# Kernel optimization log

Hardware: AMD Instinct MI355X
Metric: run time of the kernel (lower is better)

## Reference

```python
import jax, jax.numpy as jnp
import numpy as np

N_NODES = 10000
N_EDGES = 160000
D_IN = 50
ALPHA = 0.2  # LeakyReLU negative slope


def _xavier(key, shape):
    fan_in, fan_out = shape[0], int(np.prod(shape[1:]))
    limit = float(np.sqrt(6.0 / (fan_in + fan_out)))
    return jax.random.uniform(key, shape, jnp.float32, -limit, limit)


def setup_inputs() -> dict:
    key = jax.random.key(0)
    ks = jax.random.split(key, 8)
    x = jax.random.normal(ks[0], (N_NODES, D_IN), jnp.float32)
    edge_idx = jax.random.randint(ks[1], (2, N_EDGES), 0, N_NODES, jnp.int64)
    # layer 1: 50 -> 4 heads x 256, concat
    W1 = _xavier(ks[2], (D_IN, 4, 256))
    a1 = _xavier(ks[3], (4, 512))  # [H, 2F]: split into a_src, a_dst
    # layer 2: 1024 -> 4 heads x 256, concat
    W2 = _xavier(ks[4], (1024, 4, 256))
    a2 = _xavier(ks[5], (4, 512))
    # layer 3: 1024 -> 6 heads x 121, mean
    W3 = _xavier(ks[6], (1024, 6, 121))
    a3 = _xavier(ks[7], (6, 242))
    return {"x": x, "edge_idx": edge_idx, "W1": W1, "a1": a1,
            "W2": W2, "a2": a2, "W3": W3, "a3": a3}


def gat_layer(h, W, a, src, dst, aggregate):
    """Multi-head GAT layer over an edge list. h:[N,Din], W:[Din,H,F], a:[H,2F]."""
    N = h.shape[0]
    Wh = jnp.einsum('nd,dhf->nhf', h, W)                    # [N, H, F]
    F = Wh.shape[-1]
    att_src = jnp.einsum('nhf,hf->nh', Wh, a[:, :F])         # a^T [Wh_i || .]
    att_dst = jnp.einsum('nhf,hf->nh', Wh, a[:, F:])         # a^T [. || Wh_j]
    logits = jax.nn.leaky_relu(att_src[src] + att_dst[dst], ALPHA)  # [E, H]
    # numerically stable softmax over incoming edges of each destination node
    m = jax.ops.segment_max(logits, dst, num_segments=N)
    e = jnp.exp(logits - m[dst])
    denom = jax.ops.segment_sum(e, dst, num_segments=N)
    coef = e / (denom[dst] + 1e-16)                           # [E, H]
    out = jax.ops.segment_sum(coef[:, :, None] * Wh[src], dst, num_segments=N)
    if aggregate == 'concat':
        return out.reshape(N, -1)
    return out.mean(axis=1)


def reference(x, edge_idx, W1, a1, W2, a2, W3, a3):
    src, dst = edge_idx[0], edge_idx[1]
    h1 = jax.nn.elu(gat_layer(x, W1, a1, src, dst, 'concat'))   # [N, 1024]
    h2 = jax.nn.elu(gat_layer(h1, W2, a2, src, dst, 'concat'))  # [N, 1024]
    h3_in = h1 + h2                                              # residual skip
    return gat_layer(h3_in, W3, a3, src, dst, 'mean')            # [N, 121]
```

## Files before the change

kernel.cpp:

```cpp
#include <hip/hip_runtime.h>
#include <hip/hip_bf16.h>
#include <math.h>

#define NN 10000
#define NE 160000

typedef __attribute__((ext_vector_type(8))) _Float16 f16x8;
typedef __attribute__((ext_vector_type(4))) _Float16 f16x4;
typedef __attribute__((ext_vector_type(4))) float f32x4;

static __device__ __forceinline__ void gload_lds16(const _Float16* g, _Float16* l) {
  __builtin_amdgcn_global_load_lds((const __attribute__((address_space(1))) char*)g,
                                   (__attribute__((address_space(3))) char*)l, 16, 0, 0);
}

__global__ __launch_bounds__(1024) void scan_kernel(const int* __restrict__ counts,
                                                    int* __restrict__ row_ptr,
                                                    int* __restrict__ cursor, int N) {
  __shared__ int sums[1024];
  int t = threadIdx.x;
  const int CH = (N + 1023) >> 10;
  int base = t * CH;
  int s = 0;
  for (int i = 0; i < CH; ++i) { int idx = base + i; if (idx < N) s += counts[idx]; }
  sums[t] = s;
  __syncthreads();
  for (int off = 1; off < 1024; off <<= 1) {
    int v = 0;
    if (t >= off) v = sums[t - off];
    __syncthreads();
    if (t >= off) sums[t] += v;
    __syncthreads();
  }
  int run = (t == 0) ? 0 : sums[t - 1];
  for (int i = 0; i < CH; ++i) {
    int idx = base + i;
    if (idx < N) { row_ptr[idx] = run; cursor[idx] = run; run += counts[idx]; }
  }
  if (t == 0) row_ptr[N] = sums[1023];
}

__global__ void scatter_kernel(const int* __restrict__ src, const int* __restrict__ dst,
                               int* __restrict__ cursor, int* __restrict__ ssrc, int E) {
  int e = blockIdx.x * blockDim.x + threadIdx.x;
  if (e < E) {
    int pos = atomicAdd(&cursor[dst[e]], 1);
    ssrc[pos] = src[e];
  }
}

#define TB_W2 256
#define TB_W3 192
#define TB_W1 16
#define TB_T (TB_W2 + TB_W3 + TB_W1)
#define TB_X ((NN * 64) / 256)
#define TB_E ((NE + 255) / 256)
__global__ __launch_bounds__(256) void prep2(const float* __restrict__ x,
                                             const float* __restrict__ W1,
                                             const float* __restrict__ W2,
                                             const float* __restrict__ W3,
                                             const int* __restrict__ dst,
                                             int* __restrict__ counts,
                                             _Float16* __restrict__ xh,
                                             _Float16* __restrict__ w1,
                                             _Float16* __restrict__ w2,
                                             _Float16* __restrict__ w3) {
  int b = blockIdx.x;
  int t = threadIdx.x;
  if (b < TB_T) {
    const float* S;
    _Float16* D;
    int K, Nsrc, KP, k0, n0;
    if (b < TB_W2) {
      S = W2; D = w2; K = 1024; Nsrc = 1024; KP = 1024;
      k0 = (b & 15) * 64; n0 = (b >> 4) * 64;
    } else if (b < TB_W2 + TB_W3) {
      int bb = b - TB_W2;
      S = W3; D = w3; K = 1024; Nsrc = 726; KP = 1024;
      k0 = (bb & 15) * 64; n0 = (bb >> 4) * 64;
    } else {
      int bb = b - TB_W2 - TB_W3;
      S = W1; D = w1; K = 50; Nsrc = 1024; KP = 64;
      k0 = 0; n0 = bb * 64;
    }
    __shared__ float tile[64][65];
#pragma unroll
    for (int i = 0; i < 16; ++i) {
      int idx = i * 256 + t;
      int r = idx >> 6, c = idx & 63;
      int gk = k0 + r, gn = n0 + c;
      tile[r][c] = (gk < K && gn < Nsrc) ? S[(size_t)gk * Nsrc + gn] : 0.f;
    }
    __syncthreads();
#pragma unroll
    for (int i = 0; i < 16; ++i) {
      int idx = i * 256 + t;
      int r = idx >> 6, c = idx & 63;
      D[(size_t)(n0 + r) * KP + k0 + c] = (_Float16)tile[c][r];
    }
    return;
  }
  int i = (b - TB_T) * 256 + t;
  if (i < NN * 64) {
    int m = i >> 6, k = i & 63;
    xh[i] = (_Float16)(k < 50 ? x[m * 50 + k] : 0.f);
    return;
  }
  i -= NN * 64;
  if (i < NE) atomicAdd(&counts[dst[i]], 1);
}

template<int PAD121>
__global__ __launch_bounds__(256) void gemm_f16(const _Float16* __restrict__ A,
                                                const _Float16* __restrict__ B,
                                                _Float16* __restrict__ C,
                                                int M, int KP, int NC) {
  int flat = blockIdx.x;
  int xcd = flat & 7;
  int slot = flat >> 3;
  int cblk = slot % NC;
  int rblk = (slot / NC) * 8 + xcd;
  const int m0 = rblk * 128;
  if (m0 >= M) return;
  const int n0 = cblk * 128;

  __shared__ _Float16 As[128 * 64];
  __shared__ _Float16 Bs[128 * 64];

  const int t = threadIdx.x;
  const int lane = t & 63;
  const int wid = t >> 6;
  const int wr = wid >> 1;
  const int wc = wid & 1;
  const int row_in = lane & 15;
  const int kgrp = lane >> 4;

  const int srow = wid * 32 + ((lane >> 3) & 7);
  const int sl7 = lane & 7;

  f32x4 acc[4][4];
#pragma unroll
  for (int i = 0; i < 4; ++i)
#pragma unroll
    for (int j = 0; j < 4; ++j) acc[i][j] = (f32x4){0.f, 0.f, 0.f, 0.f};

  for (int k0 = 0; k0 < KP; k0 += 64) {
    if (k0) __syncthreads();
#pragma unroll
    for (int j = 0; j < 4; ++j) {
      int row = srow + j * 8;
      int gs = (sl7 ^ (row & 7)) * 8;
      int gm = m0 + row;
      if (gm >= M) gm = M - 1;
      _Float16* ldsA = &As[(wid * 32 + j * 8) * 64];
      _Float16* ldsB = &Bs[(wid * 32 + j * 8) * 64];
      gload_lds16(&A[(size_t)gm * KP + k0 + gs], ldsA);
      gload_lds16(&B[(size_t)(n0 + row) * KP + k0 + gs], ldsB);
    }
    __syncthreads();

#pragma unroll
    for (int ks = 0; ks < 2; ++ks) {
      f16x8 a[4], b[4];
#pragma unroll
      for (int mi = 0; mi < 4; ++mi) {
        int arow = wr * 64 + mi * 16 + row_in;
        int ps = ((kgrp + ks * 4) ^ (arow & 7)) * 8;
        a[mi] = *(const f16x8*)&As[arow * 64 + ps];
      }
#pragma unroll
      for (int ni = 0; ni < 4; ++ni) {
        int brow = wc * 64 + ni * 16 + row_in;
        int ps = ((kgrp + ks * 4) ^ (brow & 7)) * 8;
        b[ni] = *(const f16x8*)&Bs[brow * 64 + ps];
      }
#pragma unroll
      for (int mi = 0; mi < 4; ++mi)
#pragma unroll
        for (int ni = 0; ni < 4; ++ni)
          acc[mi][ni] = __builtin_amdgcn_mfma_f32_16x16x32_f16(a[mi], b[ni], acc[mi][ni], 0, 0, 0);
    }
  }

#pragma unroll
  for (int mi = 0; mi < 4; ++mi) {
#pragma unroll
    for (int ni = 0; ni < 4; ++ni) {
      int gn = n0 + wc * 64 + ni * 16 + row_in;
#pragma unroll
      for (int j = 0; j < 4; ++j) {
        int gm = m0 + wr * 64 + mi * 16 + kgrp * 4 + j;
        if (gm >= M) continue;
        if (PAD121) {
          if (gn < 726) {
            int h = gn / 121;
            int pc = h * 128 + (gn - h * 121);
            C[(size_t)gm * 768 + pc] = (_Float16)acc[mi][ni][j];
          }
        } else {
          C[(size_t)gm * 1024 + gn] = (_Float16)acc[mi][ni][j];
        }
      }
    }
  }
}

template<int H, int F, int SW, int HS>
__global__ void att_kernel(const _Float16* __restrict__ Whb, const float* __restrict__ a,
                           float* __restrict__ att_s, float* __restrict__ att_d, int N) {
  int n = blockIdx.x;
  int h = threadIdx.x >> 6;
  int lane = threadIdx.x & 63;
  const _Float16* w = Whb + (size_t)n * SW + h * HS;
  const float* as = a + (size_t)h * 2 * F;
  const float* ad = as + F;
  float ss = 0.f, sd = 0.f;
  if (F == 256) {
    f16x4 wv = *(const f16x4*)&w[lane * 4];
    f32x4 av = *(const f32x4*)&as[lane * 4];
    f32x4 dv = *(const f32x4*)&ad[lane * 4];
#pragma unroll
    for (int j = 0; j < 4; ++j) {
      float v = (float)wv[j];
      ss += v * av[j];
      sd += v * dv[j];
    }
  } else {
    for (int f = lane; f < F; f += 64) {
      float v = (float)w[f];
      ss += v * as[f];
      sd += v * ad[f];
    }
  }
#pragma unroll
  for (int off = 32; off > 0; off >>= 1) {
    ss += __shfl_down(ss, off);
    sd += __shfl_down(sd, off);
  }
  if (lane == 0) {
    att_s[n * H + h] = ss;
    att_d[n * H + h] = sd;
  }
}

template<int H>
__global__ __launch_bounds__(256) void edge_softmax_csr(const int* __restrict__ row_ptr,
                                                        const int* __restrict__ ssrc,
                                                        const float* __restrict__ att_s,
                                                        const float* __restrict__ att_d,
                                                        float* __restrict__ cbuf,
                                                        float* __restrict__ dinv, int N) {
  int n = blockIdx.x * 16 + (threadIdx.x >> 4);
  if (n >= N) return;
  int lane = threadIdx.x & 15;
  int beg = row_ptr[n], end = row_ptr[n + 1];

  float ad[H];
  if (H == 4) {
    f32x4 v = *(const f32x4*)&att_d[n * 4];
    ad[0] = v.x; ad[1] = v.y; ad[2] = v.z; ad[3] = v.w;
  } else {
#pragma unroll
    for (int h = 0; h < H; ++h) ad[h] = att_d[n * H + h];
  }

  float m[H];
#pragma unroll
  for (int h = 0; h < H; ++h) m[h] = -1e30f;
  for (int k = beg + lane; k < end; k += 16) {
    int s = ssrc[k];
    float as[H];
    if (H == 4) {
      f32x4 v = *(const f32x4*)&att_s[s * 4];
      as[0] = v.x; as[1] = v.y; as[2] = v.z; as[3] = v.w;
    } else {
#pragma unroll
      for (int h = 0; h < H; ++h) as[h] = att_s[s * H + h];
    }
#pragma unroll
    for (int h = 0; h < H; ++h) {
      float xv = as[h] + ad[h];
      float l = xv >= 0.f ? xv : 0.2f * xv;
      m[h] = fmaxf(m[h], l);
    }
  }
#pragma unroll
  for (int h = 0; h < H; ++h)
#pragma unroll
    for (int off = 8; off > 0; off >>= 1) m[h] = fmaxf(m[h], __shfl_xor(m[h], off));

  float sum[H];
#pragma unroll
  for (int h = 0; h < H; ++h) sum[h] = 0.f;
  for (int k = beg + lane; k < end; k += 16) {
    int s = ssrc[k];
    float as[H];
    if (H == 4) {
      f32x4 v = *(const f32x4*)&att_s[s * 4];
      as[0] = v.x; as[1] = v.y; as[2] = v.z; as[3] = v.w;
    } else {
#pragma unroll
      for (int h = 0; h < H; ++h) as[h] = att_s[s * H + h];
    }
    float ev[H];
#pragma unroll
    for (int h = 0; h < H; ++h) {
      float xv = as[h] + ad[h];
      float l = xv >= 0.f ? xv : 0.2f * xv;
      ev[h] = __expf(l - m[h]);
      sum[h] += ev[h];
    }
    if (H == 4) {
      *(f32x4*)&cbuf[(size_t)k * 4] = (f32x4){ev[0], ev[1], ev[2], ev[3]};
    } else {
#pragma unroll
      for (int h = 0; h < H; ++h) cbuf[(size_t)k * H + h] = ev[h];
    }
  }
#pragma unroll
  for (int h = 0; h < H; ++h) {
#pragma unroll
    for (int off = 8; off > 0; off >>= 1) sum[h] += __shfl_xor(sum[h], off);
  }
  if (lane < H) dinv[n * H + lane] = 1.f / (sum[lane] + 1e-16f);
}

template<int MODE>
__global__ __launch_bounds__(256) void aggregate_cat_chunk(const int* __restrict__ row_ptr,
                                                           const int* __restrict__ ssrc,
                                                           const float* __restrict__ cbuf,
                                                           const float* __restrict__ dinv,
                                                           const _Float16* __restrict__ Whb,
                                                           const _Float16* __restrict__ h1,
                                                           _Float16* __restrict__ outv, int N) {
  int b = blockIdx.x;
  int chunk = b & 7;
  int group = b >> 3;
  int n = group * 16 + (threadIdx.x >> 4);
  if (n >= N) return;
  int tt = threadIdx.x & 15;
  int idx = chunk * 128 + tt * 8;
  int h = chunk >> 1;
  float inv = dinv[n * 4 + h];

  float acc[8] = {};
  int beg = row_ptr[n], end = row_ptr[n + 1];
  int k = beg;
  for (; k + 3 < end; k += 4) {
    int s0 = ssrc[k], s1 = ssrc[k + 1], s2 = ssrc[k + 2], s3 = ssrc[k + 3];
    float c0 = cbuf[(size_t)k * 4 + h];
    float c1 = cbuf[(size_t)(k + 1) * 4 + h];
    float c2 = cbuf[(size_t)(k + 2) * 4 + h];
    float c3 = cbuf[(size_t)(k + 3) * 4 + h];
    f16x8 w0 = *(const f16x8*)&Whb[(size_t)s0 * 1024 + idx];
    f16x8 w1 = *(const f16x8*)&Whb[(size_t)s1 * 1024 + idx];
    f16x8 w2 = *(const f16x8*)&Whb[(size_t)s2 * 1024 + idx];
    f16x8 w3 = *(const f16x8*)&Whb[(size_t)s3 * 1024 + idx];
#pragma unroll
    for (int j = 0; j < 8; ++j) {
      acc[j] += c0 * (float)w0[j];
      acc[j] += c1 * (float)w1[j];
      acc[j] += c2 * (float)w2[j];
      acc[j] += c3 * (float)w3[j];
    }
  }
  for (; k < end; ++k) {
    int s0 = ssrc[k];
    float c0 = cbuf[(size_t)k * 4 + h];
    f16x8 w0 = *(const f16x8*)&Whb[(size_t)s0 * 1024 + idx];
#pragma unroll
    for (int j = 0; j < 8; ++j) acc[j] += c0 * (float)w0[j];
  }

  size_t o = (size_t)n * 1024 + idx;
  f16x8 r1;
  if (MODE == 1) r1 = *(const f16x8*)&h1[o];
  f16x8 vo;
#pragma unroll
  for (int j = 0; j < 8; ++j) {
    float v = acc[j] * inv;
    v = v > 0.f ? v : expm1f(v);
    if (MODE == 1) v += (float)r1[j];
    vo[j] = (_Float16)v;
  }
  *(f16x8*)&outv[o] = vo;
}

__global__ __launch_bounds__(256) void aggregate_mean_chunk(const int* __restrict__ row_ptr,
                                                            const int* __restrict__ ssrc,
                                                            const float* __restrict__ cbuf,
                                                            const float* __restrict__ dinv,
                                                            const _Float16* __restrict__ Whb,
                                                            float* __restrict__ part, int N) {
  int b = blockIdx.x;
  int h = b & 7;
  if (h >= 6) return;
  int n = (b >> 3) * 16 + (threadIdx.x >> 4);
  if (n >= N) return;
  int tt = threadIdx.x & 15;
  int base = h * 128 + tt * 8;
  float inv = dinv[n * 6 + h];

  float acc[8] = {};
  int beg = row_ptr[n], end = row_ptr[n + 1];
  int k = beg;
  for (; k + 3 < end; k += 4) {
    int s0 = ssrc[k], s1 = ssrc[k + 1], s2 = ssrc[k + 2], s3 = ssrc[k + 3];
    float c0 = cbuf[(size_t)k * 6 + h];
    float c1 = cbuf[(size_t)(k + 1) * 6 + h];
    float c2 = cbuf[(size_t)(k + 2) * 6 + h];
    float c3 = cbuf[(size_t)(k + 3) * 6 + h];
    f16x8 w0 = *(const f16x8*)&Whb[(size_t)s0 * 768 + base];
    f16x8 w1 = *(const f16x8*)&Whb[(size_t)s1 * 768 + base];
    f16x8 w2 = *(const f16x8*)&Whb[(size_t)s2 * 768 + base];
    f16x8 w3 = *(const f16x8*)&Whb[(size_t)s3 * 768 + base];
#pragma unroll
    for (int j = 0; j < 8; ++j) {
      acc[j] += c0 * (float)w0[j];
      acc[j] += c1 * (float)w1[j];
      acc[j] += c2 * (float)w2[j];
      acc[j] += c3 * (float)w3[j];
    }
  }
  for (; k < end; ++k) {
    int s0 = ssrc[k];
    float c0 = cbuf[(size_t)k * 6 + h];
    f16x8 w0 = *(const f16x8*)&Whb[(size_t)s0 * 768 + base];
#pragma unroll
    for (int j = 0; j < 8; ++j) acc[j] += c0 * (float)w0[j];
  }

  float* p = &part[(size_t)n * 768 + base];
  *(f32x4*)&p[0] = (f32x4){acc[0] * inv, acc[1] * inv, acc[2] * inv, acc[3] * inv};
  *(f32x4*)&p[4] = (f32x4){acc[4] * inv, acc[5] * inv, acc[6] * inv, acc[7] * inv};
}

__global__ __launch_bounds__(128) void reduce_mean(const float* __restrict__ part,
                                                   float* __restrict__ out, int N) {
  int n = blockIdx.x;
  int f = threadIdx.x;
  if (f >= 121) return;
  const float* p = &part[(size_t)n * 768];
  float s = 0.f;
#pragma unroll
  for (int h = 0; h < 6; ++h) s += p[h * 128 + f];
  out[(size_t)n * 121 + f] = s * (1.0f / 6.0f);
}

extern "C" void kernel_launch(void* const* d_in, const int* in_sizes, int n_in,
                              void* d_out, int out_size, void* d_ws, size_t ws_size,
                              hipStream_t stream) {
  const float* x  = (const float*)d_in[0];
  const int* eidx = (const int*)d_in[1];
  const float* W1 = (const float*)d_in[2];
  const float* a1 = (const float*)d_in[3];
  const float* W2 = (const float*)d_in[4];
  const float* a2 = (const float*)d_in[5];
  const float* W3 = (const float*)d_in[6];
  const float* a3 = (const float*)d_in[7];
  float* out = (float*)d_out;

  const int N = NN, E = NE;
  const int* src = eidx;
  const int* dst = eidx + E;

  char* ws = (char*)d_ws;
  size_t off = 0;
  auto alloc = [&](size_t bytes) -> void* {
    void* p = ws + off;
    off += (bytes + 255) & ~(size_t)255;
    return p;
  };
  _Float16* Whf  = (_Float16*)alloc((size_t)N * 1024 * 2);
  _Float16* h1   = (_Float16*)alloc((size_t)N * 1024 * 2);
  _Float16* hsum = (_Float16*)alloc((size_t)N * 1024 * 2);
  _Float16* xh   = (_Float16*)alloc((size_t)N * 64 * 2);
  _Float16* w1   = (_Float16*)alloc((size_t)1024 * 64 * 2);
  _Float16* w2   = (_Float16*)alloc((size_t)1024 * 1024 * 2);
  _Float16* w3   = (_Float16*)alloc((size_t)768 * 1024 * 2);
  float* cbuf  = (float*)alloc((size_t)E * 6 * 4);
  float* part  = (float*)alloc((size_t)N * 768 * 4);
  float* atts  = (float*)alloc((size_t)N * 6 * 4);
  float* attd  = (float*)alloc((size_t)N * 6 * 4);
  float* dinv  = (float*)alloc((size_t)N * 6 * 4);
  int* counts  = (int*)alloc((size_t)N * 4);
  int* row_ptr = (int*)alloc((size_t)(N + 1) * 4);
  int* cursor  = (int*)alloc((size_t)N * 4);
  int* ssrc    = (int*)alloc((size_t)E * 4);

  hipMemsetAsync(counts, 0, (size_t)N * 4, stream);
  prep2<<<TB_T + TB_X + TB_E, 256, 0, stream>>>(x, W1, W2, W3, dst, counts, xh, w1, w2, w3);
  scan_kernel<<<1, 1024, 0, stream>>>(counts, row_ptr, cursor, N);
  scatter_kernel<<<(E + 255) / 256, 256, 0, stream>>>(src, dst, cursor, ssrc, E);

  const int RPG = 10;
  const int AGG_GRID = 8 * ((N + 15) / 16);
  const int SM_GRID = (N + 15) / 16;

  gemm_f16<0><<<8 * RPG * 8, 256, 0, stream>>>(xh, w1, Whf, N, 64, 8);
  att_kernel<4, 256, 1024, 256><<<N, 256, 0, stream>>>(Whf, a1, atts, attd, N);
  edge_softmax_csr<4><<<SM_GRID, 256, 0, stream>>>(row_ptr, ssrc, atts, attd, cbuf, dinv, N);
  aggregate_cat_chunk<0><<<AGG_GRID, 256, 0, stream>>>(row_ptr, ssrc, cbuf, dinv, Whf, nullptr, h1, N);

  gemm_f16<0><<<8 * RPG * 8, 256, 0, stream>>>(h1, w2, Whf, N, 1024, 8);
  att_kernel<4, 256, 1024, 256><<<N, 256, 0, stream>>>(Whf, a2, atts, attd, N);
  edge_softmax_csr<4><<<SM_GRID, 256, 0, stream>>>(row_ptr, ssrc, atts, attd, cbuf, dinv, N);
  aggregate_cat_chunk<1><<<AGG_GRID, 256, 0, stream>>>(row_ptr, ssrc, cbuf, dinv, Whf, h1, hsum, N);

  gemm_f16<1><<<8 * RPG * 6, 256, 0, stream>>>(hsum, w3, Whf, N, 1024, 6);
  att_kernel<6, 121, 768, 128><<<N, 384, 0, stream>>>(Whf, a3, atts, attd, N);
  edge_softmax_csr<6><<<SM_GRID, 256, 0, stream>>>(row_ptr, ssrc, atts, attd, cbuf, dinv, N);
  aggregate_mean_chunk<<<AGG_GRID, 256, 0, stream>>>(row_ptr, ssrc, cbuf, dinv, Whf, part, N);
  reduce_mean<<<N, 128, 0, stream>>>(part, out, N);
}
```

Measured before the change: 273.0 us.

## Split each node's edge list across four 16-lane quarters in aggregation kernels

The aggregation kernels now give each destination node a full 64-lane wavefront instead of 16 lanes. The four 16-lane quarters process interleaved edges (stride 4) and combine their partial sums with cross-lane shuffles before one quarter writes the output. This is meant to raise memory-level parallelism and shorten the per-node serial gather loop. In exchange it launches four times as many blocks, adds shuffle reductions, and leaves three quarters of the lanes idle during the epilogue.

```diff
diff --git a/kernel.cpp b/kernel.cpp
--- a/kernel.cpp
+++ b/kernel.cpp
@@ -336,22 +336,24 @@
   int b = blockIdx.x;
   int chunk = b & 7;
   int group = b >> 3;
-  int n = group * 16 + (threadIdx.x >> 4);
+  int n = group * 4 + (threadIdx.x >> 6);
   if (n >= N) return;
-  int tt = threadIdx.x & 15;
+  int l64 = threadIdx.x & 63;
+  int quarter = l64 >> 4;
+  int tt = l64 & 15;
   int idx = chunk * 128 + tt * 8;
   int h = chunk >> 1;
   float inv = dinv[n * 4 + h];
 
   float acc[8] = {};
   int beg = row_ptr[n], end = row_ptr[n + 1];
-  int k = beg;
-  for (; k + 3 < end; k += 4) {
-    int s0 = ssrc[k], s1 = ssrc[k + 1], s2 = ssrc[k + 2], s3 = ssrc[k + 3];
+  int k = beg + quarter;
+  for (; k + 12 < end; k += 16) {
+    int s0 = ssrc[k], s1 = ssrc[k + 4], s2 = ssrc[k + 8], s3 = ssrc[k + 12];
     float c0 = cbuf[(size_t)k * 4 + h];
-    float c1 = cbuf[(size_t)(k + 1) * 4 + h];
-    float c2 = cbuf[(size_t)(k + 2) * 4 + h];
-    float c3 = cbuf[(size_t)(k + 3) * 4 + h];
+    float c1 = cbuf[(size_t)(k + 4) * 4 + h];
+    float c2 = cbuf[(size_t)(k + 8) * 4 + h];
+    float c3 = cbuf[(size_t)(k + 12) * 4 + h];
     f16x8 w0 = *(const f16x8*)&Whb[(size_t)s0 * 1024 + idx];
     f16x8 w1 = *(const f16x8*)&Whb[(size_t)s1 * 1024 + idx];
     f16x8 w2 = *(const f16x8*)&Whb[(size_t)s2 * 1024 + idx];
@@ -364,26 +366,33 @@
       acc[j] += c3 * (float)w3[j];
     }
   }
-  for (; k < end; ++k) {
+  for (; k < end; k += 4) {
     int s0 = ssrc[k];
     float c0 = cbuf[(size_t)k * 4 + h];
     f16x8 w0 = *(const f16x8*)&Whb[(size_t)s0 * 1024 + idx];
 #pragma unroll
     for (int j = 0; j < 8; ++j) acc[j] += c0 * (float)w0[j];
   }
-
-  size_t o = (size_t)n * 1024 + idx;
-  f16x8 r1;
-  if (MODE == 1) r1 = *(const f16x8*)&h1[o];
-  f16x8 vo;
 #pragma unroll
   for (int j = 0; j < 8; ++j) {
-    float v = acc[j] * inv;
-    v = v > 0.f ? v : expm1f(v);
-    if (MODE == 1) v += (float)r1[j];
-    vo[j] = (_Float16)v;
-  }
-  *(f16x8*)&outv[o] = vo;
+    acc[j] += __shfl_xor(acc[j], 16);
+    acc[j] += __shfl_xor(acc[j], 32);
+  }
+
+  if (quarter == 0) {
+    size_t o = (size_t)n * 1024 + idx;
+    f16x8 r1;
+    if (MODE == 1) r1 = *(const f16x8*)&h1[o];
+    f16x8 vo;
+#pragma unroll
+    for (int j = 0; j < 8; ++j) {
+      float v = acc[j] * inv;
+      v = v > 0.f ? v : expm1f(v);
+      if (MODE == 1) v += (float)r1[j];
+      vo[j] = (_Float16)v;
+    }
+    *(f16x8*)&outv[o] = vo;
+  }
 }
 
 __global__ __launch_bounds__(256) void aggregate_mean_chunk(const int* __restrict__ row_ptr,
@@ -395,21 +404,23 @@
   int b = blockIdx.x;
   int h = b & 7;
   if (h >= 6) return;
-  int n = (b >> 3) * 16 + (threadIdx.x >> 4);
+  int n = (b >> 3) * 4 + (threadIdx.x >> 6);
   if (n >= N) return;
-  int tt = threadIdx.x & 15;
+  int l64 = threadIdx.x & 63;
+  int quarter = l64 >> 4;
+  int tt = l64 & 15;
   int base = h * 128 + tt * 8;
   float inv = dinv[n * 6 + h];
 
   float acc[8] = {};
   int beg = row_ptr[n], end = row_ptr[n + 1];
-  int k = beg;
-  for (; k + 3 < end; k += 4) {
-    int s0 = ssrc[k], s1 = ssrc[k + 1], s2 = ssrc[k + 2], s3 = ssrc[k + 3];
+  int k = beg + quarter;
+  for (; k + 12 < end; k += 16) {
+    int s0 = ssrc[k], s1 = ssrc[k + 4], s2 = ssrc[k + 8], s3 = ssrc[k + 12];
     float c0 = cbuf[(size_t)k * 6 + h];
-    float c1 = cbuf[(size_t)(k + 1) * 6 + h];
-    float c2 = cbuf[(size_t)(k + 2) * 6 + h];
-    float c3 = cbuf[(size_t)(k + 3) * 6 + h];
+    float c1 = cbuf[(size_t)(k + 4) * 6 + h];
+    float c2 = cbuf[(size_t)(k + 8) * 6 + h];
+    float c3 = cbuf[(size_t)(k + 12) * 6 + h];
     f16x8 w0 = *(const f16x8*)&Whb[(size_t)s0 * 768 + base];
     f16x8 w1 = *(const f16x8*)&Whb[(size_t)s1 * 768 + base];
     f16x8 w2 = *(const f16x8*)&Whb[(size_t)s2 * 768 + base];
@@ -422,17 +433,24 @@
       acc[j] += c3 * (float)w3[j];
     }
   }
-  for (; k < end; ++k) {
+  for (; k < end; k += 4) {
     int s0 = ssrc[k];
     float c0 = cbuf[(size_t)k * 6 + h];
     f16x8 w0 = *(const f16x8*)&Whb[(size_t)s0 * 768 + base];
 #pragma unroll
     for (int j = 0; j < 8; ++j) acc[j] += c0 * (float)w0[j];
   }
-
-  float* p = &part[(size_t)n * 768 + base];
-  *(f32x4*)&p[0] = (f32x4){acc[0] * inv, acc[1] * inv, acc[2] * inv, acc[3] * inv};
-  *(f32x4*)&p[4] = (f32x4){acc[4] * inv, acc[5] * inv, acc[6] * inv, acc[7] * inv};
+#pragma unroll
+  for (int j = 0; j < 8; ++j) {
+    acc[j] += __shfl_xor(acc[j], 16);
+    acc[j] += __shfl_xor(acc[j], 32);
+  }
+
+  if (quarter == 0) {
+    float* p = &part[(size_t)n * 768 + base];
+    *(f32x4*)&p[0] = (f32x4){acc[0] * inv, acc[1] * inv, acc[2] * inv, acc[3] * inv};
+    *(f32x4*)&p[4] = (f32x4){acc[4] * inv, acc[5] * inv, acc[6] * inv, acc[7] * inv};
+  }
 }
 
 __global__ __launch_bounds__(128) void reduce_mean(const float* __restrict__ part,
@@ -494,7 +512,7 @@
   scatter_kernel<<<(E + 255) / 256, 256, 0, stream>>>(src, dst, cursor, ssrc, E);
 
   const int RPG = 10;
-  const int AGG_GRID = 8 * ((N + 15) / 16);
+  const int AGG_GRID = 8 * ((N + 3) / 4);
   const int SM_GRID = (N + 15) / 16;
 
   gemm_f16<0><<<8 * RPG * 8, 256, 0, stream>>>(xh, w1, Whf, N, 64, 8);
```

Result: slower. 293.2 us (+7.4%).
